# Kernel tuning notes

Measured on AMD Instinct MI355X. Metric: run time of the kernel, lower is better.

Reference implementation:

```python
import jax, jax.numpy as jnp
import numpy as np
import math

B, S, D, H = 4, 2048, 1024, 16
HD = D // H  # 64
FF = 4096
EPS = 1e-5


def layer_norm(x, g, b):
    mu = jnp.mean(x, axis=-1, keepdims=True)
    var = jnp.mean(jnp.square(x - mu), axis=-1, keepdims=True)
    return (x - mu) * jax.lax.rsqrt(var + EPS) * g + b


def setup_inputs() -> dict:
    key = jax.random.key(0)
    ks = jax.random.split(key, 16)
    sc = 0.02
    return {
        "x": jax.random.normal(ks[0], (B, S, D), dtype=jnp.float32),
        "Wq": jax.random.normal(ks[1], (H, D, HD), dtype=jnp.float32) * sc,
        "bq": jnp.zeros((H, HD), dtype=jnp.float32),
        "Wk": jax.random.normal(ks[2], (H, D, HD), dtype=jnp.float32) * sc,
        "bk": jnp.zeros((H, HD), dtype=jnp.float32),
        "Wv": jax.random.normal(ks[3], (H, D, HD), dtype=jnp.float32) * sc,
        "bv": jnp.zeros((H, HD), dtype=jnp.float32),
        "Wo": jax.random.normal(ks[4], (D, D), dtype=jnp.float32) * sc,
        "bo": jnp.zeros((D,), dtype=jnp.float32),
        "W1": jax.random.normal(ks[5], (D, FF), dtype=jnp.float32) * sc,
        "b1": jnp.zeros((FF,), dtype=jnp.float32),
        "W2": jax.random.normal(ks[6], (FF, D), dtype=jnp.float32) * sc,
        "b2": jnp.zeros((D,), dtype=jnp.float32),
        "ln1_g": jnp.ones((D,), dtype=jnp.float32),
        "ln1_b": jnp.zeros((D,), dtype=jnp.float32),
        "ln2_g": jnp.ones((D,), dtype=jnp.float32),
        "ln2_b": jnp.zeros((D,), dtype=jnp.float32),
    }


def reference(x, Wq, bq, Wk, bk, Wv, bv, Wo, bo, W1, b1, W2, b2, ln1_g, ln1_b, ln2_g, ln2_b):
    b, s, d = x.shape
    h1 = layer_norm(x, ln1_g, ln1_b)
    # per-head Q/K/V linears, vectorized over heads: [b,h,s,hd]
    q = jnp.einsum('bsd,hde->bhse', h1, Wq) + bq[None, :, None, :]
    k = jnp.einsum('bsd,hde->bhse', h1, Wk) + bk[None, :, None, :]
    v = jnp.einsum('bsd,hde->bhse', h1, Wv) + bv[None, :, None, :]
    scores = jnp.einsum('bhqe,bhke->bhqk', q, k) / math.sqrt(q.shape[-1])
    causal = jnp.tril(jnp.ones((s, s), dtype=bool))
    scores = jnp.where(causal[None, None], scores, -jnp.inf)
    weights = jax.nn.softmax(scores, axis=-1)
    attn = jnp.einsum('bhqk,bhke->bhqe', weights, v)
    # concat heads (head order = torch concat dim=-1)
    attn = attn.transpose(0, 2, 1, 3).reshape(b, s, d)
    x = x + attn @ Wo + bo
    h2 = layer_norm(x, ln2_g, ln2_b)
    y = jax.nn.gelu(h2 @ W1 + b1, approximate=False)
    y = jax.nn.gelu(y @ W2 + b2, approximate=False)
    return x + y
```

## Files before the change

kernel.cpp:

```cpp
#include <hip/hip_runtime.h>
#include <cstdint>
#include <cstddef>


#define DI __device__ __forceinline__

typedef __attribute__((ext_vector_type(8))) __bf16 bf16x8;
typedef __attribute__((ext_vector_type(4))) float floatx4;

static constexpr int Bn = 4, Sn = 2048, Dn = 1024, Hn = 16, HDn = 64, FFn = 4096;
static constexpr int NTOK = Bn * Sn;
static constexpr int D3 = 3 * Dn;

DI float bf2f(unsigned short u) { return __uint_as_float(((unsigned int)u) << 16); }
DI unsigned short f2bf(float f) {
  unsigned int u = __float_as_uint(f);
  u += 0x7FFFu + ((u >> 16) & 1u);
  return (unsigned short)(u >> 16);
}
DI float gelu_f(float v) { return 0.5f * v * (1.0f + erff(v * 0.70710678118654752f)); }
DI bf16x8 ld8(const unsigned short* p) { return *(const bf16x8*)p; }
DI floatx4 mfma16(bf16x8 a, bf16x8 b, floatx4 c) {
  return __builtin_amdgcn_mfma_f32_16x16x32_bf16(a, b, c, 0, 0, 0);
}
DI void g2l16(const unsigned short* g, unsigned short* l) {
  __builtin_amdgcn_global_load_lds((__attribute__((address_space(1))) void*)g,
                                   (__attribute__((address_space(3))) void*)l,
                                   16, 0, 0);
}
DI float ldin(const void* p, size_t idx, bool f32) {
  return f32 ? ((const float*)p)[idx] : bf2f(((const unsigned short*)p)[idx]);
}
DI int swz16(int row, int col) {
  return (row << 6) + ((((col >> 3) ^ row ^ (row >> 3)) & 7) << 3) + (col & 7);
}

__global__ void detect_kernel(const unsigned short* __restrict__ x,
                              int* __restrict__ flag) {
  int t = threadIdx.x;
  int cnt = 0;
  for (int i = t; i < 1024; i += 64) {
    unsigned short u = x[2 * i];
    int e = (u >> 7) & 0xFF;
    cnt += (e >= 96 && e <= 142) ? 1 : 0;
  }
  #pragma unroll
  for (int off = 32; off >= 1; off >>= 1) cnt += __shfl_xor(cnt, off);
  if (t == 0) *flag = (cnt < 820) ? 1 : 0;
}

__global__ void vec_prep(const void* bq, const void* bk, const void* bv,
                         const void* bo, const void* b1, const void* b2,
                         const void* g1, const void* be1, const void* g2,
                         const void* be2, unsigned short* __restrict__ dst,
                         const int* __restrict__ flag) {
  int i = blockIdx.x * 256 + threadIdx.x;
  if (i >= 13312) return;
  const bool f32 = *flag != 0;
  const void* src; int off;
  if      (i < 1024)  { src = bq;  off = i; }
  else if (i < 2048)  { src = bk;  off = i - 1024; }
  else if (i < 3072)  { src = bv;  off = i - 2048; }
  else if (i < 4096)  { src = bo;  off = i - 3072; }
  else if (i < 8192)  { src = b1;  off = i - 4096; }
  else if (i < 9216)  { src = b2;  off = i - 8192; }
  else if (i < 10240) { src = g1;  off = i - 9216; }
  else if (i < 11264) { src = be1; off = i - 10240; }
  else if (i < 12288) { src = g2;  off = i - 11264; }
  else                { src = be2; off = i - 12288; }
  dst[i] = f2bf(ldin(src, off, f32));
}

__global__ void transpose_kernel(const void* __restrict__ src,
                                 unsigned short* __restrict__ dst, int K, int N,
                                 const int* __restrict__ flag) {
  __shared__ unsigned short tile[64][65];
  const bool f32 = *flag != 0;
  int kb = blockIdx.y * 64, nb = blockIdx.x * 64;
  for (int i = threadIdx.x; i < 4096; i += 256) {
    int r = i >> 6, c = i & 63;
    tile[r][c] = f2bf(ldin(src, (size_t)(kb + r) * N + nb + c, f32));
  }
  __syncthreads();
  for (int i = threadIdx.x; i < 4096; i += 256) {
    int r = i >> 6, c = i & 63;
    dst[(size_t)(nb + r) * K + kb + c] = tile[c][r];
  }
}

__global__ void qkvT_kernel(const void* __restrict__ Wq,
                            const void* __restrict__ Wk,
                            const void* __restrict__ Wv,
                            unsigned short* __restrict__ WT,
                            const int* __restrict__ flag) {
  __shared__ unsigned short tile[64][65];
  const bool f32 = *flag != 0;
  const void* src = blockIdx.z == 0 ? Wq : (blockIdx.z == 1 ? Wk : Wv);
  int h = blockIdx.y, d0 = blockIdx.x * 64;
  size_t base = (size_t)h * (Dn * HDn);
  for (int i = threadIdx.x; i < 4096; i += 256) {
    int r = i >> 6, c = i & 63;
    tile[r][c] = f2bf(ldin(src, base + (size_t)(d0 + r) * 64 + c, f32));
  }
  __syncthreads();
  for (int i = threadIdx.x; i < 4096; i += 256) {
    int r = i >> 6, c = i & 63;
    WT[(size_t)(blockIdx.z * 1024 + h * 64 + r) * 1024 + d0 + c] = tile[c][r];
  }
}

__global__ __launch_bounds__(256) void ln_kernel(const void* __restrict__ x,
                                                 const unsigned short* __restrict__ g,
                                                 const unsigned short* __restrict__ b,
                                                 unsigned short* __restrict__ out,
                                                 const int* __restrict__ flag) {
  const bool f32 = flag ? (*flag != 0) : true;
  int row = blockIdx.x, t = threadIdx.x;
  float v[4];
  if (f32) {
    float4 f = *(const float4*)((const float*)x + (size_t)row * Dn + t * 4);
    v[0] = f.x; v[1] = f.y; v[2] = f.z; v[3] = f.w;
  } else {
    ushort4 u = *(const ushort4*)((const unsigned short*)x + (size_t)row * Dn + t * 4);
    v[0] = bf2f(u.x); v[1] = bf2f(u.y); v[2] = bf2f(u.z); v[3] = bf2f(u.w);
  }
  float s = v[0] + v[1] + v[2] + v[3];
  float s2 = v[0] * v[0] + v[1] * v[1] + v[2] * v[2] + v[3] * v[3];
  #pragma unroll
  for (int off = 32; off >= 1; off >>= 1) {
    s += __shfl_xor(s, off);
    s2 += __shfl_xor(s2, off);
  }
  __shared__ float red[8];
  int wv = t >> 6, ln = t & 63;
  if (ln == 0) { red[wv] = s; red[4 + wv] = s2; }
  __syncthreads();
  s = red[0] + red[1] + red[2] + red[3];
  s2 = red[4] + red[5] + red[6] + red[7];
  float mu = s * (1.0f / 1024.0f);
  float var = s2 * (1.0f / 1024.0f) - mu * mu;
  float rs = rsqrtf(fmaxf(var, 0.0f) + 1e-5f);
  ushort4 gg = *(const ushort4*)(g + t * 4);
  ushort4 bb = *(const ushort4*)(b + t * 4);
  ushort4 o;
  o.x = f2bf((v[0] - mu) * rs * bf2f(gg.x) + bf2f(bb.x));
  o.y = f2bf((v[1] - mu) * rs * bf2f(gg.y) + bf2f(bb.y));
  o.z = f2bf((v[2] - mu) * rs * bf2f(gg.z) + bf2f(bb.z));
  o.w = f2bf((v[3] - mu) * rs * bf2f(gg.w) + bf2f(bb.w));
  *(ushort4*)(out + (size_t)row * Dn + t * 4) = o;
}

enum { EPI_BIAS_BF16 = 0, EPI_WO = 1, EPI_GELU = 2, EPI_FF2 = 3 };

template <int EPI>
__global__ __launch_bounds__(256, 3) void gemm_kernel(
    const unsigned short* __restrict__ A, const unsigned short* __restrict__ BT,
    const unsigned short* __restrict__ bias, const void* __restrict__ residv,
    const float* __restrict__ resid_f, unsigned short* __restrict__ Cb,
    float* __restrict__ Cf, const int* __restrict__ flag, int M, int N, int K) {
  __shared__ unsigned short As[128 * 32];
  __shared__ unsigned short Bs[128 * 32];
  const int m0 = blockIdx.y * 128, n0 = blockIdx.x * 128;
  const int w = threadIdx.x >> 6, lane = threadIdx.x & 63;
  const int waveM = (w >> 1) * 64, waveN = (w & 1) * 64;
  const int m16 = lane & 15, quad = lane >> 4;
  const bool rf32 = flag && (*flag != 0);

  const int srow = w * 32 + (lane >> 2);
  const int scol = (lane & 3) * 8;
  const unsigned short* Ag = A + (size_t)(m0 + srow) * K + scol;
  const unsigned short* Bg = BT + (size_t)(n0 + srow) * K + scol;
  unsigned short* Al = As + srow * 32 + scol;
  unsigned short* Bl = Bs + srow * 32 + scol;
  const size_t rowstep = (size_t)16 * K;

  floatx4 acc[4][4];
  #pragma unroll
  for (int i = 0; i < 4; i++)
    #pragma unroll
    for (int j = 0; j < 4; j++) acc[i][j] = floatx4{0.f, 0.f, 0.f, 0.f};

  for (int k0 = 0; k0 < K; k0 += 32) {
    g2l16(Ag, Al);
    g2l16(Ag + rowstep, Al + 16 * 32);
    g2l16(Bg, Bl);
    g2l16(Bg + rowstep, Bl + 16 * 32);
    Ag += 32; Bg += 32;
    __syncthreads();
    bf16x8 af[4], bfv[4];
    #pragma unroll
    for (int mt = 0; mt < 4; mt++)
      af[mt] = ld8(As + (waveM + mt * 16 + m16) * 32 + quad * 8);
    #pragma unroll
    for (int nt = 0; nt < 4; nt++)
      bfv[nt] = ld8(Bs + (waveN + nt * 16 + m16) * 32 + quad * 8);
    #pragma unroll
    for (int mt = 0; mt < 4; mt++)
      #pragma unroll
      for (int nt = 0; nt < 4; nt++)
        acc[mt][nt] = mfma16(af[mt], bfv[nt], acc[mt][nt]);
    __syncthreads();
  }

  #pragma unroll
  for (int mt = 0; mt < 4; mt++) {
    #pragma unroll
    for (int nt = 0; nt < 4; nt++) {
      const int col = n0 + waveN + nt * 16 + m16;
      const float bcol = bf2f(bias[col]);
      #pragma unroll
      for (int r = 0; r < 4; r++) {
        const int row = m0 + waveM + mt * 16 + quad * 4 + r;
        const size_t idx = (size_t)row * N + col;
        float v = acc[mt][nt][r] + bcol;
        if constexpr (EPI == EPI_BIAS_BF16) {
          Cb[idx] = f2bf(v);
        } else if constexpr (EPI == EPI_WO) {
          float rv = rf32 ? ((const float*)residv)[idx]
                          : bf2f(((const unsigned short*)residv)[idx]);
          Cf[idx] = v + rv;
        } else if constexpr (EPI == EPI_GELU) {
          Cb[idx] = f2bf(gelu_f(v));
        } else {
          float ov = gelu_f(v) + resid_f[idx];
          if (rf32) Cf[idx] = ov;
          else      Cb[idx] = f2bf(ov);
        }
      }
    }
  }
}

__global__ __launch_bounds__(256, 4) void attn_kernel(
    const unsigned short* __restrict__ qkv, unsigned short* __restrict__ attn) {
  const int qt = (int)gridDim.x - 1 - (int)blockIdx.x;
  const int bh = blockIdx.y;
  const int b = bh >> 4, h = bh & 15;
  const int tid = threadIdx.x;
  const int w = tid >> 6, lane = tid & 63;
  const int m16 = lane & 15, quad = lane >> 4;

  __shared__ unsigned short Ks[2][4096];
  __shared__ unsigned short Vt[2][4096];
  __shared__ unsigned short Ps[4][1024];
  unsigned short* PsW = Ps[w];

  const int qrow = qt * 64 + w * 16 + m16;
  const unsigned short* qp = qkv + (size_t)(b * Sn + qrow) * D3 + h * 64 + quad * 8;
  const bf16x8 qf0 = ld8(qp), qf1 = ld8(qp + 32);

  floatx4 acc_o[4];
  #pragma unroll
  for (int nt = 0; nt < 4; nt++) acc_o[nt] = floatx4{0.f, 0.f, 0.f, 0.f};
  float lsum[4] = {0.f, 0.f, 0.f, 0.f};

  const int kr = tid >> 3, kc = (tid & 7) * 8;
  const int vk = (tid >> 3) * 2, ve = (tid & 7) * 8;

  uint4 kreg0, kreg1, vreg0, vreg1;
  const unsigned short* const kvroot = qkv + (size_t)(b * Sn) * D3 + h * 64;

  {
    const unsigned short* base = kvroot;
    kreg0 = *(const uint4*)(base + (size_t)kr * D3 + 1024 + kc);
    kreg1 = *(const uint4*)(base + (size_t)(kr + 32) * D3 + 1024 + kc);
    vreg0 = *(const uint4*)(base + (size_t)vk * D3 + 2048 + ve);
    vreg1 = *(const uint4*)(base + (size_t)(vk + 1) * D3 + 2048 + ve);
  }

  for (int kt = 0; kt <= qt; ++kt) {
    const int pb = kt & 1;
    *(uint4*)(Ks[pb] + swz16(kr, kc)) = kreg0;
    *(uint4*)(Ks[pb] + swz16(kr + 32, kc)) = kreg1;
    {
      const unsigned short* a0 = (const unsigned short*)&vreg0;
      const unsigned short* a1 = (const unsigned short*)&vreg1;
      #pragma unroll
      for (int i = 0; i < 8; i++) {
        unsigned int word = (unsigned int)a0[i] | ((unsigned int)a1[i] << 16);
        *(unsigned int*)(Vt[pb] + swz16(ve + i, vk)) = word;
      }
    }
    __syncthreads();
    if (kt < qt) {
      const unsigned short* base = kvroot + (size_t)(kt + 1) * 64 * D3;
      kreg0 = *(const uint4*)(base + (size_t)kr * D3 + 1024 + kc);
      kreg1 = *(const uint4*)(base + (size_t)(kr + 32) * D3 + 1024 + kc);
      vreg0 = *(const uint4*)(base + (size_t)vk * D3 + 2048 + ve);
      vreg1 = *(const uint4*)(base + (size_t)(vk + 1) * D3 + 2048 + ve);
    }

    floatx4 sa[4];
    #pragma unroll
    for (int nt = 0; nt < 4; nt++) {
      bf16x8 k0 = ld8(Ks[pb] + swz16(nt * 16 + m16, quad * 8));
      bf16x8 k1 = ld8(Ks[pb] + swz16(nt * 16 + m16, 32 + quad * 8));
      floatx4 t = mfma16(qf0, k0, floatx4{0.f, 0.f, 0.f, 0.f});
      sa[nt] = mfma16(qf1, k1, t);
    }

    #pragma unroll
    for (int r = 0; r < 4; r++) {
      const int qgr = qt * 64 + w * 16 + quad * 4 + r;
      #pragma unroll
      for (int nt = 0; nt < 4; nt++) {
        const int kgc = kt * 64 + nt * 16 + m16;
        float pv = (kgc <= qgr) ? __expf(sa[nt][r] * 0.125f) : 0.0f;
        lsum[r] += pv;
        PsW[swz16(quad * 4 + r, nt * 16 + m16)] = f2bf(pv);
      }
    }
    const bf16x8 p0 = ld8(PsW + swz16(m16, quad * 8));
    const bf16x8 p1 = ld8(PsW + swz16(m16, 32 + quad * 8));
    #pragma unroll
    for (int nt = 0; nt < 4; nt++) {
      bf16x8 v0 = ld8(Vt[pb] + swz16(nt * 16 + m16, quad * 8));
      bf16x8 v1 = ld8(Vt[pb] + swz16(nt * 16 + m16, 32 + quad * 8));
      acc_o[nt] = mfma16(p0, v0, acc_o[nt]);
      acc_o[nt] = mfma16(p1, v1, acc_o[nt]);
    }
  }

  #pragma unroll
  for (int r = 0; r < 4; r++) {
    #pragma unroll
    for (int off = 1; off < 16; off <<= 1) lsum[r] += __shfl_xor(lsum[r], off);
  }

  #pragma unroll
  for (int r = 0; r < 4; r++) {
    const float inv = 1.0f / fmaxf(lsum[r], 1e-20f);
    const size_t orow = (size_t)(b * Sn + qt * 64 + w * 16 + quad * 4 + r) * Dn + h * 64;
    #pragma unroll
    for (int nt = 0; nt < 4; nt++)
      attn[orow + nt * 16 + m16] = f2bf(acc_o[nt][r] * inv);
  }
}

extern "C" void kernel_launch(void* const* d_in, const int* in_sizes, int n_in,
                              void* d_out, int out_size, void* d_ws, size_t ws_size,
                              hipStream_t stream) {
  (void)in_sizes; (void)n_in; (void)out_size; (void)ws_size;
  const void* x    = d_in[0];
  const void* Wq   = d_in[1];
  const void* bq   = d_in[2];
  const void* Wk   = d_in[3];
  const void* bk   = d_in[4];
  const void* Wv   = d_in[5];
  const void* bv   = d_in[6];
  const void* Wo   = d_in[7];
  const void* bo   = d_in[8];
  const void* W1   = d_in[9];
  const void* b1   = d_in[10];
  const void* W2   = d_in[11];
  const void* b2   = d_in[12];
  const void* ln1g = d_in[13];
  const void* ln1b = d_in[14];
  const void* ln2g = d_in[15];
  const void* ln2b = d_in[16];
  char* ws = (char*)d_ws;

  constexpr size_t OFF_WTQKV = 0;
  constexpr size_t OFF_WOT   = OFF_WTQKV + (size_t)D3 * Dn * 2;
  constexpr size_t OFF_W1T   = OFF_WOT + (size_t)Dn * Dn * 2;
  constexpr size_t OFF_W2T   = OFF_W1T + (size_t)FFn * Dn * 2;
  constexpr size_t OFF_VEC   = OFF_W2T + (size_t)Dn * FFn * 2;
  constexpr size_t OFF_FLAG  = OFF_VEC + 32768;
  constexpr size_t OFF_H     = OFF_FLAG + 256;
  constexpr size_t OFF_QKV   = OFF_H + (size_t)NTOK * Dn * 2;
  constexpr size_t OFF_ATTN  = OFF_QKV + (size_t)NTOK * D3 * 2;
  constexpr size_t OFF_X2    = OFF_ATTN + (size_t)NTOK * Dn * 2;
  constexpr size_t OFF_Y1    = OFF_QKV;

  unsigned short* WTqkv = (unsigned short*)(ws + OFF_WTQKV);
  unsigned short* WoT   = (unsigned short*)(ws + OFF_WOT);
  unsigned short* W1T   = (unsigned short*)(ws + OFF_W1T);
  unsigned short* W2T   = (unsigned short*)(ws + OFF_W2T);
  unsigned short* vec   = (unsigned short*)(ws + OFF_VEC);
  int*            flag  = (int*)(ws + OFF_FLAG);
  unsigned short* hbuf  = (unsigned short*)(ws + OFF_H);
  unsigned short* qkvb  = (unsigned short*)(ws + OFF_QKV);
  unsigned short* attnb = (unsigned short*)(ws + OFF_ATTN);
  float*          x2    = (float*)(ws + OFF_X2);
  unsigned short* y1    = (unsigned short*)(ws + OFF_Y1);

  detect_kernel<<<1, 64, 0, stream>>>((const unsigned short*)x, flag);

  vec_prep<<<52, 256, 0, stream>>>(bq, bk, bv, bo, b1, b2, ln1g, ln1b, ln2g,
                                   ln2b, vec, flag);
  qkvT_kernel<<<dim3(16, 16, 3), 256, 0, stream>>>(Wq, Wk, Wv, WTqkv, flag);
  transpose_kernel<<<dim3(16, 16), 256, 0, stream>>>(Wo, WoT, 1024, 1024, flag);
  transpose_kernel<<<dim3(64, 16), 256, 0, stream>>>(W1, W1T, 1024, 4096, flag);
  transpose_kernel<<<dim3(16, 64), 256, 0, stream>>>(W2, W2T, 4096, 1024, flag);

  ln_kernel<<<NTOK, 256, 0, stream>>>(x, vec + 9216, vec + 10240, hbuf, flag);
  gemm_kernel<EPI_BIAS_BF16><<<dim3(D3 / 128, NTOK / 128), 256, 0, stream>>>(
      hbuf, WTqkv, vec + 0, nullptr, nullptr, qkvb, nullptr, nullptr,
      NTOK, D3, Dn);
  attn_kernel<<<dim3(Sn / 64, Bn * Hn), 256, 0, stream>>>(qkvb, attnb);
  gemm_kernel<EPI_WO><<<dim3(Dn / 128, NTOK / 128), 256, 0, stream>>>(
      attnb, WoT, vec + 3072, x, nullptr, nullptr, x2, flag, NTOK, Dn, Dn);
  ln_kernel<<<NTOK, 256, 0, stream>>>(x2, vec + 11264, vec + 12288, hbuf, nullptr);
  gemm_kernel<EPI_GELU><<<dim3(FFn / 128, NTOK / 128), 256, 0, stream>>>(
      hbuf, W1T, vec + 4096, nullptr, nullptr, y1, nullptr, nullptr,
      NTOK, FFn, Dn);
  gemm_kernel<EPI_FF2><<<dim3(Dn / 128, NTOK / 128), 256, 0, stream>>>(
      y1, W2T, vec + 8192, nullptr, x2, (unsigned short*)d_out, (float*)d_out,
      flag, NTOK, Dn, FFn);
}
```

Baseline: 667.8 us.

## Enlarge attention query tile to 128 rows and interleave causal block order

The attention kernel now handles 128 query rows per block (two 16-row MFMA tiles per wave), so each K/V tile loaded into shared memory serves twice as many queries, halving K/V traffic per query. Block indices are interleaved so long and short causal rows alternate for better load balance, and exp is computed via exp2f with a pre-scaled constant. The GEMM launch bound is relaxed from 3 to 2 blocks per SM, giving the compiler more registers at the cost of occupancy. The larger tile raises register pressure in attention and halves the grid size.

```diff
diff --git a/kernel.cpp b/kernel.cpp
--- a/kernel.cpp
+++ b/kernel.cpp
@@ -153,7 +153,7 @@
 enum { EPI_BIAS_BF16 = 0, EPI_WO = 1, EPI_GELU = 2, EPI_FF2 = 3 };
 
 template <int EPI>
-__global__ __launch_bounds__(256, 3) void gemm_kernel(
+__global__ __launch_bounds__(256, 2) void gemm_kernel(
     const unsigned short* __restrict__ A, const unsigned short* __restrict__ BT,
     const unsigned short* __restrict__ bias, const void* __restrict__ residv,
     const float* __restrict__ resid_f, unsigned short* __restrict__ Cb,
@@ -233,7 +233,8 @@
 
 __global__ __launch_bounds__(256, 4) void attn_kernel(
     const unsigned short* __restrict__ qkv, unsigned short* __restrict__ attn) {
-  const int qt = (int)gridDim.x - 1 - (int)blockIdx.x;
+  const int i = (int)blockIdx.x;
+  const int qt = (i & 1) ? (i >> 1) : (15 - (i >> 1));
   const int bh = blockIdx.y;
   const int b = bh >> 4, h = bh & 15;
   const int tid = threadIdx.x;
@@ -245,14 +246,25 @@
   __shared__ unsigned short Ps[4][1024];
   unsigned short* PsW = Ps[w];
 
-  const int qrow = qt * 64 + w * 16 + m16;
-  const unsigned short* qp = qkv + (size_t)(b * Sn + qrow) * D3 + h * 64 + quad * 8;
-  const bf16x8 qf0 = ld8(qp), qf1 = ld8(qp + 32);
-
-  floatx4 acc_o[4];
-  #pragma unroll
-  for (int nt = 0; nt < 4; nt++) acc_o[nt] = floatx4{0.f, 0.f, 0.f, 0.f};
-  float lsum[4] = {0.f, 0.f, 0.f, 0.f};
+  bf16x8 qf[2][2];
+  #pragma unroll
+  for (int mt = 0; mt < 2; mt++) {
+    const int qrow = qt * 128 + w * 32 + mt * 16 + m16;
+    const unsigned short* qp =
+        qkv + (size_t)(b * Sn + qrow) * D3 + h * 64 + quad * 8;
+    qf[mt][0] = ld8(qp);
+    qf[mt][1] = ld8(qp + 32);
+  }
+
+  floatx4 acc_o[2][4];
+  float lsum[2][4];
+  #pragma unroll
+  for (int mt = 0; mt < 2; mt++)
+    #pragma unroll
+    for (int j = 0; j < 4; j++) {
+      acc_o[mt][j] = floatx4{0.f, 0.f, 0.f, 0.f};
+      lsum[mt][j] = 0.f;
+    }
 
   const int kr = tid >> 3, kc = (tid & 7) * 8;
   const int vk = (tid >> 3) * 2, ve = (tid & 7) * 8;
@@ -260,15 +272,14 @@
   uint4 kreg0, kreg1, vreg0, vreg1;
   const unsigned short* const kvroot = qkv + (size_t)(b * Sn) * D3 + h * 64;
 
-  {
-    const unsigned short* base = kvroot;
-    kreg0 = *(const uint4*)(base + (size_t)kr * D3 + 1024 + kc);
-    kreg1 = *(const uint4*)(base + (size_t)(kr + 32) * D3 + 1024 + kc);
-    vreg0 = *(const uint4*)(base + (size_t)vk * D3 + 2048 + ve);
-    vreg1 = *(const uint4*)(base + (size_t)(vk + 1) * D3 + 2048 + ve);
-  }
-
-  for (int kt = 0; kt <= qt; ++kt) {
+  kreg0 = *(const uint4*)(kvroot + (size_t)kr * D3 + 1024 + kc);
+  kreg1 = *(const uint4*)(kvroot + (size_t)(kr + 32) * D3 + 1024 + kc);
+  vreg0 = *(const uint4*)(kvroot + (size_t)vk * D3 + 2048 + ve);
+  vreg1 = *(const uint4*)(kvroot + (size_t)(vk + 1) * D3 + 2048 + ve);
+
+  const float ESC = 0.125f * 1.44269504088896f;
+  const int ktmax = 2 * qt + 1;
+  for (int kt = 0; kt <= ktmax; ++kt) {
     const int pb = kt & 1;
     *(uint4*)(Ks[pb] + swz16(kr, kc)) = kreg0;
     *(uint4*)(Ks[pb] + swz16(kr + 32, kc)) = kreg1;
@@ -276,13 +287,13 @@
       const unsigned short* a0 = (const unsigned short*)&vreg0;
       const unsigned short* a1 = (const unsigned short*)&vreg1;
       #pragma unroll
-      for (int i = 0; i < 8; i++) {
-        unsigned int word = (unsigned int)a0[i] | ((unsigned int)a1[i] << 16);
-        *(unsigned int*)(Vt[pb] + swz16(ve + i, vk)) = word;
+      for (int j = 0; j < 8; j++) {
+        unsigned int word = (unsigned int)a0[j] | ((unsigned int)a1[j] << 16);
+        *(unsigned int*)(Vt[pb] + swz16(ve + j, vk)) = word;
       }
     }
     __syncthreads();
-    if (kt < qt) {
+    if (kt < ktmax) {
       const unsigned short* base = kvroot + (size_t)(kt + 1) * 64 * D3;
       kreg0 = *(const uint4*)(base + (size_t)kr * D3 + 1024 + kc);
       kreg1 = *(const uint4*)(base + (size_t)(kr + 32) * D3 + 1024 + kc);
@@ -290,51 +301,68 @@
       vreg1 = *(const uint4*)(base + (size_t)(vk + 1) * D3 + 2048 + ve);
     }
 
-    floatx4 sa[4];
+    floatx4 sa[2][4];
     #pragma unroll
     for (int nt = 0; nt < 4; nt++) {
       bf16x8 k0 = ld8(Ks[pb] + swz16(nt * 16 + m16, quad * 8));
       bf16x8 k1 = ld8(Ks[pb] + swz16(nt * 16 + m16, 32 + quad * 8));
-      floatx4 t = mfma16(qf0, k0, floatx4{0.f, 0.f, 0.f, 0.f});
-      sa[nt] = mfma16(qf1, k1, t);
-    }
-
-    #pragma unroll
-    for (int r = 0; r < 4; r++) {
-      const int qgr = qt * 64 + w * 16 + quad * 4 + r;
-      #pragma unroll
-      for (int nt = 0; nt < 4; nt++) {
-        const int kgc = kt * 64 + nt * 16 + m16;
-        float pv = (kgc <= qgr) ? __expf(sa[nt][r] * 0.125f) : 0.0f;
-        lsum[r] += pv;
-        PsW[swz16(quad * 4 + r, nt * 16 + m16)] = f2bf(pv);
+      #pragma unroll
+      for (int mt = 0; mt < 2; mt++) {
+        floatx4 t = mfma16(qf[mt][0], k0, floatx4{0.f, 0.f, 0.f, 0.f});
+        sa[mt][nt] = mfma16(qf[mt][1], k1, t);
       }
     }
-    const bf16x8 p0 = ld8(PsW + swz16(m16, quad * 8));
-    const bf16x8 p1 = ld8(PsW + swz16(m16, 32 + quad * 8));
+
+    bf16x8 pf[2][2];
+    #pragma unroll
+    for (int mt = 0; mt < 2; mt++) {
+      #pragma unroll
+      for (int r = 0; r < 4; r++) {
+        const int qgr = qt * 128 + w * 32 + mt * 16 + quad * 4 + r;
+        #pragma unroll
+        for (int nt = 0; nt < 4; nt++) {
+          const int kgc = kt * 64 + nt * 16 + m16;
+          float pv = (kgc <= qgr) ? exp2f(sa[mt][nt][r] * ESC) : 0.0f;
+          lsum[mt][r] += pv;
+          PsW[swz16(quad * 4 + r, nt * 16 + m16)] = f2bf(pv);
+        }
+      }
+      pf[mt][0] = ld8(PsW + swz16(m16, quad * 8));
+      pf[mt][1] = ld8(PsW + swz16(m16, 32 + quad * 8));
+    }
     #pragma unroll
     for (int nt = 0; nt < 4; nt++) {
       bf16x8 v0 = ld8(Vt[pb] + swz16(nt * 16 + m16, quad * 8));
       bf16x8 v1 = ld8(Vt[pb] + swz16(nt * 16 + m16, 32 + quad * 8));
-      acc_o[nt] = mfma16(p0, v0, acc_o[nt]);
-      acc_o[nt] = mfma16(p1, v1, acc_o[nt]);
-    }
-  }
-
-  #pragma unroll
-  for (int r = 0; r < 4; r++) {
-    #pragma unroll
-    for (int off = 1; off < 16; off <<= 1) lsum[r] += __shfl_xor(lsum[r], off);
-  }
-
-  #pragma unroll
-  for (int r = 0; r < 4; r++) {
-    const float inv = 1.0f / fmaxf(lsum[r], 1e-20f);
-    const size_t orow = (size_t)(b * Sn + qt * 64 + w * 16 + quad * 4 + r) * Dn + h * 64;
-    #pragma unroll
-    for (int nt = 0; nt < 4; nt++)
-      attn[orow + nt * 16 + m16] = f2bf(acc_o[nt][r] * inv);
-  }
+      #pragma unroll
+      for (int mt = 0; mt < 2; mt++) {
+        acc_o[mt][nt] = mfma16(pf[mt][0], v0, acc_o[mt][nt]);
+        acc_o[mt][nt] = mfma16(pf[mt][1], v1, acc_o[mt][nt]);
+      }
+    }
+  }
+
+  #pragma unroll
+  for (int mt = 0; mt < 2; mt++)
+    #pragma unroll
+    for (int r = 0; r < 4; r++) {
+      #pragma unroll
+      for (int off = 1; off < 16; off <<= 1)
+        lsum[mt][r] += __shfl_xor(lsum[mt][r], off);
+    }
+
+  #pragma unroll
+  for (int mt = 0; mt < 2; mt++)
+    #pragma unroll
+    for (int r = 0; r < 4; r++) {
+      const float inv = 1.0f / fmaxf(lsum[mt][r], 1e-20f);
+      const size_t orow =
+          (size_t)(b * Sn + qt * 128 + w * 32 + mt * 16 + quad * 4 + r) * Dn +
+          h * 64;
+      #pragma unroll
+      for (int nt = 0; nt < 4; nt++)
+        attn[orow + nt * 16 + m16] = f2bf(acc_o[mt][nt][r] * inv);
+    }
 }
 
 extern "C" void kernel_launch(void* const* d_in, const int* in_sizes, int n_in,
@@ -397,7 +425,7 @@
   gemm_kernel<EPI_BIAS_BF16><<<dim3(D3 / 128, NTOK / 128), 256, 0, stream>>>(
       hbuf, WTqkv, vec + 0, nullptr, nullptr, qkvb, nullptr, nullptr,
       NTOK, D3, Dn);
-  attn_kernel<<<dim3(Sn / 64, Bn * Hn), 256, 0, stream>>>(qkvb, attnb);
+  attn_kernel<<<dim3(Sn / 128, Bn * Hn), 256, 0, stream>>>(qkvb, attnb);
   gemm_kernel<EPI_WO><<<dim3(Dn / 128, NTOK / 128), 256, 0, stream>>>(
       attnb, WoT, vec + 3072, x, nullptr, nullptr, x2, flag, NTOK, Dn, Dn);
   ln_kernel<<<NTOK, 256, 0, stream>>>(x2, vec + 11264, vec + 12288, hbuf, nullptr);
```

Result: slower. 992.2 us (+48.6%).
